# Performance work log

Measured on AMD Instinct MI355X. Metric: run time of the kernel, lower is better.

Reference implementation:

```python
import jax, jax.numpy as jnp
import numpy as np

B, S, D, H = 2, 2048, 1024, 16
DK = D // H


def setup_inputs() -> dict:
    key = jax.random.key(0)
    ks = jax.random.split(key, 7)
    scale = 1.0 / np.sqrt(D)
    return {
        "q": jax.random.normal(ks[0], (B, S, D), dtype=jnp.float32),
        "k": jax.random.normal(ks[1], (B, S, D), dtype=jnp.float32),
        "v": jax.random.normal(ks[2], (B, S, D), dtype=jnp.float32),
        "mask": jnp.ones((B, 1, 1, S), dtype=jnp.int32),
        "Wq": (jax.random.normal(ks[3], (D, D), dtype=jnp.float32) * scale),
        "Wk": (jax.random.normal(ks[4], (D, D), dtype=jnp.float32) * scale),
        "Wv": (jax.random.normal(ks[5], (D, D), dtype=jnp.float32) * scale),
        "Wo": (jax.random.normal(ks[6], (D, D), dtype=jnp.float32) * scale),
    }


def reference(q, k, v, mask, Wq, Wk, Wv, Wo):
    # nn.Linear(bias=False): y = x @ W.T
    def split_heads(x):  # [B,S,D] -> [B,H,S,DK]
        return x.reshape(B, S, H, DK).transpose(0, 2, 1, 3)

    qh = split_heads(q @ Wq.T)
    kh = split_heads(k @ Wk.T)
    vh = split_heads(v @ Wv.T)

    scores = jnp.einsum("bhqd,bhkd->bhqk", qh, kh) / jnp.sqrt(
        jnp.asarray(DK, dtype=qh.dtype))
    scores = jnp.where(mask == 0, jnp.asarray(-1e9, dtype=scores.dtype), scores)
    attn = jax.nn.softmax(scores, axis=-1)  # dropout p=0.0 -> identity

    ctx = jnp.einsum("bhqk,bhkd->bhqd", attn, vh)  # [B,H,S,DK]
    ctx = ctx.transpose(0, 2, 1, 3).reshape(B, S, D)
    return ctx @ Wo.T
```

## Files before the change

### kernel.cpp

```cpp
#include <hip/hip_runtime.h>


typedef __bf16 bf16x8 __attribute__((ext_vector_type(8)));
typedef __bf16 bf16x4 __attribute__((ext_vector_type(4)));
typedef float f32x4 __attribute__((ext_vector_type(4)));

#define B_ 2
#define S_ 2048
#define D_ 1024
#define H_ 16
#define DK_ 64
#define QSCALE 0.18033688011112042f

__global__ void detect_dtype(const unsigned int* __restrict__ qw,
                             int* __restrict__ flag) {
  int cnt = 0;
#pragma unroll
  for (int i = 0; i < 4; ++i) {
    unsigned int w = qw[threadIdx.x + 64 * i];
    int e = (w >> 7) & 0xFF;
    cnt += (e >= 100 && e <= 140) ? 1 : 0;
  }
#pragma unroll
  for (int off = 32; off > 0; off >>= 1) cnt += __shfl_down(cnt, off, 64);
  if (threadIdx.x == 0) *flag = (cnt >= 128) ? 0 : 1;
}

__device__ __forceinline__ bf16x8 load8cvt(const void* base, size_t eoff,
                                           bool f32) {
  if (!f32) return *(const bf16x8*)((const __bf16*)base + eoff);
  const float* p = (const float*)base + eoff;
  bf16x8 r;
#pragma unroll
  for (int j = 0; j < 8; ++j) r[j] = (__bf16)p[j];
  return r;
}

__device__ __forceinline__ void async_cp16(const __bf16* g, __bf16* l) {
  __builtin_amdgcn_global_load_lds(
      (const __attribute__((address_space(1))) unsigned int*)g,
      (__attribute__((address_space(3))) unsigned int*)l, 16, 0, 0);
}

template <int TM, int MODE>
__global__ __launch_bounds__(256) void gemmk(
    const void* X0, const void* X1, const void* X2,
    const void* W0, const void* W1, const void* W2,
    void* O0, void* O1, void* O2, const int* __restrict__ dflag) {
  constexpr int Kd = 1024, Nd = 1024;
  constexpr int NI = (TM == 128) ? 4 : 2;
  constexpr int ACH = TM / 32;
  constexpr int BCH = 4;
  const void* X = (blockIdx.z == 0) ? X0 : (blockIdx.z == 1 ? X1 : X2);
  const void* W = (blockIdx.z == 0) ? W0 : (blockIdx.z == 1 ? W1 : W2);
  void* O = (blockIdx.z == 0) ? O0 : (blockIdx.z == 1 ? O1 : O2);
  const bool f32io = (*dflag != 0);

  __shared__ __attribute__((aligned(16))) __bf16 As[TM * 64];
  __shared__ __attribute__((aligned(16))) __bf16 Bs[128 * 64];

  const int m0 = blockIdx.x * TM;
  const int n0 = blockIdx.y * 128;
  const int t = threadIdx.x;
  const int lane = t & 63, wave = t >> 6;
  const int l15 = lane & 15, quad = lane >> 4;
  const int wm = (TM == 128) ? (wave >> 1) * 64 : 0;
  const int wn = (TM == 128) ? (wave & 1) * 64 : wave * 32;

  const __bf16* gA[ACH];
  __bf16* ldsA[ACH];
#pragma unroll
  for (int i = 0; i < ACH; ++i) {
    int c = (wave * ACH + i) * 64 + lane;
    int row = c >> 3, j = c & 7;
    int jl = j ^ (row & 7);
    ldsA[i] = &As[(wave * ACH + i) * 512];
    if (MODE == 0) {
      gA[i] = (const __bf16*)X + (size_t)(m0 + row) * Kd + jl * 8;
    } else {
      int gm = m0 + row;
      gA[i] = (const __bf16*)X + (size_t)(gm >> 11) * (H_ * S_ * DK_) +
              (size_t)(gm & (S_ - 1)) * DK_ + jl * 8;
    }
  }
  const __bf16* gB[BCH];
  __bf16* ldsB[BCH];
#pragma unroll
  for (int i = 0; i < BCH; ++i) {
    int c = (wave * BCH + i) * 64 + lane;
    int row = c >> 3, j = c & 7;
    int jl = j ^ (row & 7);
    ldsB[i] = &Bs[(wave * BCH + i) * 512];
    gB[i] = (const __bf16*)W + (size_t)(n0 + row) * Kd + jl * 8;
  }

  f32x4 acc[4][NI] = {};

  for (int k0 = 0; k0 < Kd; k0 += 64) {
    __syncthreads();
    if (!f32io) {
      if (MODE == 0) {
#pragma unroll
        for (int i = 0; i < ACH; ++i) async_cp16(gA[i] + k0, ldsA[i]);
      } else {
        const size_t koff = (size_t)(k0 >> 6) * (S_ * DK_);
#pragma unroll
        for (int i = 0; i < ACH; ++i) async_cp16(gA[i] + koff, ldsA[i]);
      }
#pragma unroll
      for (int i = 0; i < BCH; ++i) async_cp16(gB[i] + k0, ldsB[i]);
    } else {
#pragma unroll
      for (int i = 0; i < TM / 32; ++i) {
        int c = t + 256 * i;
        int row = c >> 3, j = c & 7;
        int jl = j ^ (row & 7);
        bf16x8 xv;
        if (MODE == 0) {
          xv = load8cvt(X, (size_t)(m0 + row) * Kd + k0 + jl * 8, true);
        } else {
          int gm = m0 + row, gk = k0 + jl * 8;
          xv = *(const bf16x8*)((const __bf16*)X +
                ((((size_t)(gm >> 11) * H_ + (gk >> 6)) * S_) +
                 (gm & (S_ - 1))) * DK_ + (gk & (DK_ - 1)));
        }
        *(bf16x8*)&As[row * 64 + j * 8] = xv;
      }
#pragma unroll
      for (int i = 0; i < 4; ++i) {
        int c = t + 256 * i;
        int row = c >> 3, j = c & 7;
        int jl = j ^ (row & 7);
        bf16x8 wv = load8cvt(W, (size_t)(n0 + row) * Kd + k0 + jl * 8, true);
        *(bf16x8*)&Bs[row * 64 + j * 8] = wv;
      }
    }
    __syncthreads();

#pragma unroll
    for (int h = 0; h < 2; ++h) {
      bf16x8 af[4], bfr[NI];
#pragma unroll
      for (int mi = 0; mi < 4; ++mi) {
        int row = wm + mi * 16 + l15;
        af[mi] = *(const bf16x8*)&As[row * 64 +
                                     (((h * 4 + quad) ^ (row & 7)) << 3)];
      }
#pragma unroll
      for (int ni = 0; ni < NI; ++ni) {
        int row = wn + ni * 16 + l15;
        bfr[ni] = *(const bf16x8*)&Bs[row * 64 +
                                      (((h * 4 + quad) ^ (row & 7)) << 3)];
      }
#pragma unroll
      for (int mi = 0; mi < 4; ++mi)
#pragma unroll
        for (int ni = 0; ni < NI; ++ni)
          acc[mi][ni] = __builtin_amdgcn_mfma_f32_16x16x32_bf16(
              af[mi], bfr[ni], acc[mi][ni], 0, 0, 0);
    }
  }

  const float oscale = (MODE == 0 && blockIdx.z == 0) ? QSCALE : 1.0f;
#pragma unroll
  for (int mi = 0; mi < 4; ++mi) {
#pragma unroll
    for (int ni = 0; ni < NI; ++ni) {
      int mbase = m0 + wm + mi * 16 + quad * 4;
      int n = n0 + wn + ni * 16 + l15;
      if (MODE == 0 && blockIdx.z == 2) {
        int b = mbase >> 11, sb = mbase & (S_ - 1);
        int h = n >> 6, dk = n & (DK_ - 1);
        bf16x4 pk;
#pragma unroll
        for (int r = 0; r < 4; ++r) pk[r] = (__bf16)acc[mi][ni][r];
        *(bf16x4*)&((__bf16*)O)[((size_t)(b * H_ + h) * DK_ + dk) * S_ + sb] = pk;
      } else {
#pragma unroll
        for (int r = 0; r < 4; ++r) {
          int m = mbase + r;
          float val = acc[mi][ni][r] * oscale;
          if (MODE == 0) {
            int b = m >> 11, s = m & (S_ - 1);
            int h = n >> 6, dk = n & (DK_ - 1);
            ((__bf16*)O)[((size_t)(b * H_ + h) * S_ + s) * DK_ + dk] = (__bf16)val;
          } else {
            size_t idx = (size_t)m * Nd + n;
            if (f32io) ((float*)O)[idx] = val;
            else       ((__bf16*)O)[idx] = (__bf16)val;
          }
        }
      }
    }
  }
}

__global__ __launch_bounds__(256, 2) void attn(
    const __bf16* Qh, const __bf16* __restrict__ Kh,
    const __bf16* __restrict__ Vt, const int* __restrict__ mask,
    __bf16* Out) {
  __shared__ __attribute__((aligned(16))) __bf16 Ks[2][4096];
  __shared__ __attribute__((aligned(16))) __bf16 Vs[2][4096];
  __shared__ __attribute__((aligned(16))) __bf16 P[4][2048];

  const int t = threadIdx.x;
  const int lane = t & 63, wave = t >> 6;
  const int l15 = lane & 15, quad = lane >> 4;
  const int qb = blockIdx.x & 15;
  const int bh = blockIdx.x >> 4;
  const int b = bh >> 4;
  const int q0 = qb * 128 + wave * 32;

  const __bf16* Q = Qh + (size_t)bh * S_ * DK_;
  const __bf16* K = Kh + (size_t)bh * S_ * DK_;
  const __bf16* V = Vt + (size_t)bh * DK_ * S_;
  const int* mk = mask + b * S_;

  bf16x8 qf[2][2];
#pragma unroll
  for (int qt = 0; qt < 2; ++qt) {
    qf[qt][0] = *(const bf16x8*)&Q[(size_t)(q0 + qt * 16 + l15) * DK_ + quad * 8];
    qf[qt][1] = *(const bf16x8*)&Q[(size_t)(q0 + qt * 16 + l15) * DK_ + 32 + quad * 8];
  }

  f32x4 o[2][4] = {};
  float lsum[2] = {0.f, 0.f};

  int pst[4], prd[2];
#pragma unroll
  for (int tt = 0; tt < 4; ++tt)
    pst[tt] = l15 * 64 + (((tt * 2 + (quad >> 1)) ^ (l15 & 7)) << 3) +
              (quad & 1) * 4;
#pragma unroll
  for (int kt = 0; kt < 2; ++kt)
    prd[kt] = l15 * 64 + (((kt * 4 + quad) ^ (l15 & 7)) << 3);

#pragma unroll
  for (int i = 0; i < 2; ++i) {
    int l = wave * 128 + i * 64 + lane;
    int row = l >> 3, jg = (l & 7) ^ (row & 7);
    async_cp16(K + (size_t)row * DK_ + jg * 8, &Ks[0][(size_t)(l - lane) * 8]);
    async_cp16(V + (size_t)row * S_ + jg * 8, &Vs[0][(size_t)(l - lane) * 8]);
  }
  __syncthreads();

  for (int kb = 0; kb < S_; kb += 64) {
    const int cur = (kb >> 6) & 1;
    if (kb + 64 < S_) {
#pragma unroll
      for (int i = 0; i < 2; ++i) {
        int l = wave * 128 + i * 64 + lane;
        int row = l >> 3, jg = (l & 7) ^ (row & 7);
        async_cp16(K + (size_t)(kb + 64 + row) * DK_ + jg * 8,
                   &Ks[cur ^ 1][(size_t)(l - lane) * 8]);
        async_cp16(V + (size_t)row * S_ + (kb + 64) + jg * 8,
                   &Vs[cur ^ 1][(size_t)(l - lane) * 8]);
      }
    }

    const __bf16* ks = &Ks[cur][0];
    f32x4 s[2][4];
#pragma unroll
    for (int tt = 0; tt < 4; ++tt) {
      int row = tt * 16 + l15;
      bf16x8 kf0 = *(const bf16x8*)&ks[row * 64 + ((quad ^ (l15 & 7)) << 3)];
      bf16x8 kf1 = *(const bf16x8*)&ks[row * 64 + (((4 + quad) ^ (l15 & 7)) << 3)];
      int4 m4 = *(const int4*)&mk[kb + tt * 16 + quad * 4];
      f32x4 z;
      z[0] = m4.x ? 0.f : -1e9f;
      z[1] = m4.y ? 0.f : -1e9f;
      z[2] = m4.z ? 0.f : -1e9f;
      z[3] = m4.w ? 0.f : -1e9f;
      f32x4 z0 = __builtin_amdgcn_mfma_f32_16x16x32_bf16(kf0, qf[0][0], z, 0, 0, 0);
      s[0][tt] = __builtin_amdgcn_mfma_f32_16x16x32_bf16(kf1, qf[0][1], z0, 0, 0, 0);
      f32x4 z1 = __builtin_amdgcn_mfma_f32_16x16x32_bf16(kf0, qf[1][0], z, 0, 0, 0);
      s[1][tt] = __builtin_amdgcn_mfma_f32_16x16x32_bf16(kf1, qf[1][1], z1, 0, 0, 0);
    }

    const __bf16* vs = &Vs[cur][0];
    bf16x8 vf[2][4];
#pragma unroll
    for (int kt = 0; kt < 2; ++kt)
#pragma unroll
      for (int nt = 0; nt < 4; ++nt) {
        int dk = nt * 16 + l15;
        vf[kt][nt] =
            *(const bf16x8*)&vs[dk * 64 + (((kt * 4 + quad) ^ (l15 & 7)) << 3)];
      }

#pragma unroll
    for (int qt = 0; qt < 2; ++qt) {
      float acc = 0.f;
#pragma unroll
      for (int tt = 0; tt < 4; ++tt) {
        bf16x4 pk;
#pragma unroll
        for (int r = 0; r < 4; ++r) {
          float e = __builtin_exp2f(s[qt][tt][r]);
          acc += e;
          pk[r] = (__bf16)e;
        }
        *(bf16x4*)&P[wave][qt * 1024 + pst[tt]] = pk;
      }
      lsum[qt] += acc;
    }

    asm volatile("" ::: "memory");

#pragma unroll
    for (int qt = 0; qt < 2; ++qt)
#pragma unroll
      for (int kt = 0; kt < 2; ++kt) {
        bf16x8 pf = *(const bf16x8*)&P[wave][qt * 1024 + prd[kt]];
#pragma unroll
        for (int nt = 0; nt < 4; ++nt)
          o[qt][nt] = __builtin_amdgcn_mfma_f32_16x16x32_bf16(
              pf, vf[kt][nt], o[qt][nt], 0, 0, 0);
      }

    __syncthreads();
  }

#pragma unroll
  for (int qt = 0; qt < 2; ++qt) {
    float v = lsum[qt];
    v += __shfl_xor(v, 16, 64);
    v += __shfl_xor(v, 32, 64);
    lsum[qt] = v;
  }

#pragma unroll
  for (int qt = 0; qt < 2; ++qt) {
    float rinv[4];
#pragma unroll
    for (int r = 0; r < 4; ++r)
      rinv[r] = 1.0f / __shfl(lsum[qt], quad * 4 + r, 64);
#pragma unroll
    for (int nt = 0; nt < 4; ++nt)
#pragma unroll
      for (int r = 0; r < 4; ++r) {
        int qrow = q0 + qt * 16 + quad * 4 + r;
        Out[(size_t)bh * S_ * DK_ + (size_t)qrow * DK_ + nt * 16 + l15] =
            (__bf16)(o[qt][nt][r] * rinv[r]);
      }
  }
}

extern "C" void kernel_launch(void* const* d_in, const int* in_sizes, int n_in,
                              void* d_out, int out_size, void* d_ws, size_t ws_size,
                              hipStream_t stream) {
  const void* q = d_in[0];
  const void* k = d_in[1];
  const void* v = d_in[2];
  const int* mask = (const int*)d_in[3];
  const void* Wq = d_in[4];
  const void* Wk = d_in[5];
  const void* Wv = d_in[6];
  const void* Wo = d_in[7];

  const size_t NE = (size_t)B_ * H_ * S_ * DK_;
  __bf16* Qh = (__bf16*)d_ws;
  __bf16* Kh = Qh + NE;
  int* dflag = (int*)((char*)d_ws + 2 * NE * sizeof(__bf16));
  __bf16* Vt = (__bf16*)d_out;

  detect_dtype<<<1, 64, 0, stream>>>((const unsigned int*)q, dflag);
  dim3 g1(32, 8, 3);
  gemmk<128, 0><<<g1, 256, 0, stream>>>(q, k, v, Wq, Wk, Wv, Qh, Kh, Vt, dflag);
  attn<<<512, 256, 0, stream>>>(Qh, Kh, Vt, mask, Qh);
  dim3 g2(64, 8, 1);
  gemmk<64, 1><<<g2, 256, 0, stream>>>(Qh, Qh, Qh, Wo, Wo, Wo, d_out, d_out,
                                       d_out, dflag);
}
```

Baseline: 256.4 us.

## Double-buffer LDS tiles in projection GEMM to overlap loads with MFMA

Splits the GEMM's shared-memory A/B tiles into two buffers. The next K-tile is issued with async global-to-LDS copies (or the fp32 convert path) while the current tile feeds the MFMAs, and the loop drops to one barrier per iteration. The goal is to hide global load latency behind compute. In exchange LDS use doubles, which may cut occupancy, and the async copies need a wait before the barrier to be correct.

```diff
diff --git a/kernel.cpp b/kernel.cpp
--- a/kernel.cpp
+++ b/kernel.cpp
@@ -51,13 +51,15 @@
   constexpr int NI = (TM == 128) ? 4 : 2;
   constexpr int ACH = TM / 32;
   constexpr int BCH = 4;
+  constexpr int ASZ = TM * 64;
+  constexpr int BSZ = 128 * 64;
   const void* X = (blockIdx.z == 0) ? X0 : (blockIdx.z == 1 ? X1 : X2);
   const void* W = (blockIdx.z == 0) ? W0 : (blockIdx.z == 1 ? W1 : W2);
   void* O = (blockIdx.z == 0) ? O0 : (blockIdx.z == 1 ? O1 : O2);
   const bool f32io = (*dflag != 0);
 
-  __shared__ __attribute__((aligned(16))) __bf16 As[TM * 64];
-  __shared__ __attribute__((aligned(16))) __bf16 Bs[128 * 64];
+  __shared__ __attribute__((aligned(16))) __bf16 As[2][ASZ];
+  __shared__ __attribute__((aligned(16))) __bf16 Bs[2][BSZ];
 
   const int m0 = blockIdx.x * TM;
   const int n0 = blockIdx.y * 128;
@@ -68,13 +70,13 @@
   const int wn = (TM == 128) ? (wave & 1) * 64 : wave * 32;
 
   const __bf16* gA[ACH];
-  __bf16* ldsA[ACH];
+  int ldsAoff[ACH];
 #pragma unroll
   for (int i = 0; i < ACH; ++i) {
     int c = (wave * ACH + i) * 64 + lane;
     int row = c >> 3, j = c & 7;
     int jl = j ^ (row & 7);
-    ldsA[i] = &As[(wave * ACH + i) * 512];
+    ldsAoff[i] = (wave * ACH + i) * 512;
     if (MODE == 0) {
       gA[i] = (const __bf16*)X + (size_t)(m0 + row) * Kd + jl * 8;
     } else {
@@ -84,31 +86,31 @@
     }
   }
   const __bf16* gB[BCH];
-  __bf16* ldsB[BCH];
+  int ldsBoff[BCH];
 #pragma unroll
   for (int i = 0; i < BCH; ++i) {
     int c = (wave * BCH + i) * 64 + lane;
     int row = c >> 3, j = c & 7;
     int jl = j ^ (row & 7);
-    ldsB[i] = &Bs[(wave * BCH + i) * 512];
+    ldsBoff[i] = (wave * BCH + i) * 512;
     gB[i] = (const __bf16*)W + (size_t)(n0 + row) * Kd + jl * 8;
   }
 
-  f32x4 acc[4][NI] = {};
-
-  for (int k0 = 0; k0 < Kd; k0 += 64) {
-    __syncthreads();
+  auto stage_tile = [&](int k0, int bsel) {
     if (!f32io) {
       if (MODE == 0) {
 #pragma unroll
-        for (int i = 0; i < ACH; ++i) async_cp16(gA[i] + k0, ldsA[i]);
+        for (int i = 0; i < ACH; ++i)
+          async_cp16(gA[i] + k0, &As[bsel][ldsAoff[i]]);
       } else {
         const size_t koff = (size_t)(k0 >> 6) * (S_ * DK_);
 #pragma unroll
-        for (int i = 0; i < ACH; ++i) async_cp16(gA[i] + koff, ldsA[i]);
-      }
-#pragma unroll
-      for (int i = 0; i < BCH; ++i) async_cp16(gB[i] + k0, ldsB[i]);
+        for (int i = 0; i < ACH; ++i)
+          async_cp16(gA[i] + koff, &As[bsel][ldsAoff[i]]);
+      }
+#pragma unroll
+      for (int i = 0; i < BCH; ++i)
+        async_cp16(gB[i] + k0, &Bs[bsel][ldsBoff[i]]);
     } else {
 #pragma unroll
       for (int i = 0; i < TM / 32; ++i) {
@@ -124,7 +126,7 @@
                 ((((size_t)(gm >> 11) * H_ + (gk >> 6)) * S_) +
                  (gm & (S_ - 1))) * DK_ + (gk & (DK_ - 1)));
         }
-        *(bf16x8*)&As[row * 64 + j * 8] = xv;
+        *(bf16x8*)&As[bsel][row * 64 + j * 8] = xv;
       }
 #pragma unroll
       for (int i = 0; i < 4; ++i) {
@@ -132,10 +134,20 @@
         int row = c >> 3, j = c & 7;
         int jl = j ^ (row & 7);
         bf16x8 wv = load8cvt(W, (size_t)(n0 + row) * Kd + k0 + jl * 8, true);
-        *(bf16x8*)&Bs[row * 64 + j * 8] = wv;
-      }
-    }
-    __syncthreads();
+        *(bf16x8*)&Bs[bsel][row * 64 + j * 8] = wv;
+      }
+    }
+  };
+
+  f32x4 acc[4][NI] = {};
+
+  stage_tile(0, 0);
+  __syncthreads();
+
+  for (int k0 = 0; k0 < Kd; k0 += 64) {
+    const int cur = (k0 >> 6) & 1;
+    const bool more = (k0 + 64 < Kd);
+    if (more) stage_tile(k0 + 64, cur ^ 1);
 
 #pragma unroll
     for (int h = 0; h < 2; ++h) {
@@ -143,14 +155,14 @@
 #pragma unroll
       for (int mi = 0; mi < 4; ++mi) {
         int row = wm + mi * 16 + l15;
-        af[mi] = *(const bf16x8*)&As[row * 64 +
-                                     (((h * 4 + quad) ^ (row & 7)) << 3)];
+        af[mi] = *(const bf16x8*)&As[cur][row * 64 +
+                                          (((h * 4 + quad) ^ (row & 7)) << 3)];
       }
 #pragma unroll
       for (int ni = 0; ni < NI; ++ni) {
         int row = wn + ni * 16 + l15;
-        bfr[ni] = *(const bf16x8*)&Bs[row * 64 +
-                                      (((h * 4 + quad) ^ (row & 7)) << 3)];
+        bfr[ni] = *(const bf16x8*)&Bs[cur][row * 64 +
+                                           (((h * 4 + quad) ^ (row & 7)) << 3)];
       }
 #pragma unroll
       for (int mi = 0; mi < 4; ++mi)
@@ -159,6 +171,8 @@
           acc[mi][ni] = __builtin_amdgcn_mfma_f32_16x16x32_bf16(
               af[mi], bfr[ni], acc[mi][ni], 0, 0, 0);
     }
+
+    if (more) __syncthreads();
   }
 
   const float oscale = (MODE == 0 && blockIdx.z == 0) ? QSCALE : 1.0f;
```

Measured after the change: 263.0 us. 2.6% more time.
